# Performance work log

Hardware: AMD Instinct MI355X
Metric: run time of the kernel (lower is better)

Reference implementation:

```python
import jax, jax.numpy as jnp
import numpy as np

B, T = 64, 2048
RNN_DIM, EMB_DIM, ATTN_DIM = 1024, 512, 128
N_FILT, KSIZE = 32, 31
PAD = (KSIZE - 1) // 2


def setup_inputs() -> dict:
    key = jax.random.key(0)
    ks = jax.random.split(key, 8)
    s = 0.02
    return {
        "attention_hidden_state": jax.random.normal(ks[0], (B, RNN_DIM), jnp.float32),
        "memory": jax.random.normal(ks[1], (B, T, EMB_DIM), jnp.float32),
        "processed_memory": jax.random.normal(ks[2], (B, T, ATTN_DIM), jnp.float32),
        "attention_weights_cat": jax.random.uniform(ks[3], (B, 2, T), jnp.float32),
        "mask": jnp.zeros((B, T), dtype=bool),
        "Wq": jax.random.normal(ks[4], (ATTN_DIM, RNN_DIM), jnp.float32) * s,
        "Wconv": jax.random.normal(ks[5], (N_FILT, 2, KSIZE), jnp.float32) * s,
        "Wloc": jax.random.normal(ks[6], (ATTN_DIM, N_FILT), jnp.float32) * s,
        "Wv": jax.random.normal(ks[7], (1, ATTN_DIM), jnp.float32) * s,
    }


def reference(attention_hidden_state, memory, processed_memory,
              attention_weights_cat, mask, Wq, Wconv, Wloc, Wv):
    # query projection: [B, rnn] -> [B, 1, attn]
    pq = jnp.einsum("br,ar->ba", attention_hidden_state, Wq)[:, None, :]
    # location conv: [B, 2, T] -> [B, F, T]
    conv = jax.lax.conv_general_dilated(
        attention_weights_cat, Wconv, window_strides=(1,),
        padding=[(PAD, PAD)], dimension_numbers=("NCH", "OIH", "NCH"))
    # [B, T, F] @ Wloc.T -> [B, T, attn]
    ploc = jnp.einsum("bft,af->bta", conv, Wloc)
    # energies: [B, T]
    energies = jnp.einsum("bta,oa->bto", jnp.tanh(pq + ploc + processed_memory), Wv)[..., 0]
    alignment = jnp.where(mask, -jnp.inf, energies)
    attention_weights = jax.nn.softmax(alignment, axis=1)
    # context: [B, emb]
    attention_context = jnp.einsum("bt,bte->be", attention_weights, memory)
    return attention_context, attention_weights
```

## Files before the change

### kernel.cpp

```cpp
#include <hip/hip_runtime.h>
#include <math.h>

#define BB 64
#define TT 2048
#define RNN 1024
#define EMB 512
#define ATTN 128
#define NF 32
#define KS 31
#define PADW 15

#define TCHK_BLK 128
#define TCHK_W 32
#define NCH (TT / TCHK_W)

__device__ __forceinline__ float fast_tanh(float x) {
    float ax = fabsf(x);
    float e = __expf(-2.f * ax);
    float r = (1.f - e) * __builtin_amdgcn_rcpf(1.f + e);
    return copysignf(r, x);
}

__global__ __launch_bounds__(256) void pq_kernel(const float* __restrict__ h,
                                                 const float* __restrict__ Wq,
                                                 float* __restrict__ pq) {
    int b = blockIdx.x >> 2;
    int q = blockIdx.x & 3;
    __shared__ float s_h[RNN];
    for (int i = threadIdx.x; i < RNN; i += 256) s_h[i] = h[b * RNN + i];
    __syncthreads();

    int wave = threadIdx.x >> 6;
    int lane = threadIdx.x & 63;
#pragma unroll 2
    for (int j = 0; j < 8; ++j) {
        int a = q * 32 + wave * 8 + j;
        const float4* wq4 = (const float4*)(Wq + (size_t)a * RNN);
        float acc = 0.f;
#pragma unroll
        for (int i = 0; i < 4; ++i) {
            float4 w4 = wq4[lane + 64 * i];
            float4 h4 = *(const float4*)(s_h + 4 * (lane + 64 * i));
            acc += w4.x * h4.x + w4.y * h4.y + w4.z * h4.z + w4.w * h4.w;
        }
#pragma unroll
        for (int off = 32; off > 0; off >>= 1) acc += __shfl_xor(acc, off, 64);
        if (lane == 0) pq[b * ATTN + a] = acc;
    }
}

__global__ __launch_bounds__(256) void fused2_kernel(
    const float* __restrict__ pm,
    const float* __restrict__ awc,
    const float* __restrict__ mem,
    const unsigned char* __restrict__ mask,
    const float* __restrict__ pq,
    const float* __restrict__ Wconv,
    const float* __restrict__ Wloc,
    const float* __restrict__ Wv,
    float* __restrict__ wp,
    float* __restrict__ ms,
    float* __restrict__ cp)
{
    int b = blockIdx.x >> 4;
    int blk = blockIdx.x & 15;
    int t0b = blk * TCHK_BLK;
    int tid = threadIdx.x;
    int w = tid >> 6;
    int l = tid & 63;
    int tpair = l >> 1;
    int ah = l & 1;
    int t_local = w * TCHK_W + tpair;
    int tg = t0b + t_local;
    int ch = blk * 4 + w;
    int t0w = t0b + w * TCHK_W;

    __shared__ float s_awc[2][TCHK_BLK + 2 * PADW + 2];
    __shared__ float s_wl[ATTN * NF];
    __shared__ float s_pq[ATTN];
    __shared__ float s_wv[ATTN];
    __shared__ float s_p[4][TCHK_W];

    for (int i = tid; i < 2 * (TCHK_BLK + 2 * PADW); i += 256) {
        int c = i / (TCHK_BLK + 2 * PADW);
        int j = i % (TCHK_BLK + 2 * PADW);
        int tgj = t0b - PADW + j;
        s_awc[c][j] = (tgj >= 0 && tgj < TT) ? awc[((size_t)b * 2 + c) * TT + tgj] : 0.f;
    }
#pragma unroll
    for (int i = 0; i < 4; ++i)
        ((float4*)s_wl)[tid + 256 * i] = ((const float4*)Wloc)[tid + 256 * i];
    if (tid < ATTN) {
        s_pq[tid] = pq[b * ATTN + tid];
        s_wv[tid] = Wv[tid];
    }
    __syncthreads();

    float c_[NF];
    {
        float aw[KS];
#pragma unroll
        for (int k = 0; k < KS; ++k) aw[k] = s_awc[0][t_local + k];
#pragma unroll
        for (int f = 0; f < NF; ++f) {
            float acc = 0.f;
#pragma unroll
            for (int k = 0; k < KS; ++k)
                acc += aw[k] * Wconv[(f * 2 + 0) * KS + k];
            c_[f] = acc;
        }
#pragma unroll
        for (int k = 0; k < KS; ++k) aw[k] = s_awc[1][t_local + k];
#pragma unroll
        for (int f = 0; f < NF; ++f) {
            float acc = c_[f];
#pragma unroll
            for (int k = 0; k < KS; ++k)
                acc += aw[k] * Wconv[(f * 2 + 1) * KS + k];
            c_[f] = acc;
        }
    }

    int a0 = ah * 64;
    const float4* pm4 = (const float4*)(pm + ((size_t)b * TT + tg) * ATTN + a0);
    float epart = 0.f;

    auto enA = [&](int a_rel, float pmc) {
        int a = a0 + a_rel;
        const float4* wl4 = (const float4*)&s_wl[a << 5];
        float v = s_pq[a] + pmc;
#pragma unroll
        for (int f4 = 0; f4 < 8; ++f4) {
            float4 wq = wl4[f4];
            v += c_[f4 * 4 + 0] * wq.x + c_[f4 * 4 + 1] * wq.y +
                 c_[f4 * 4 + 2] * wq.z + c_[f4 * 4 + 3] * wq.w;
        }
        epart += s_wv[a] * fast_tanh(v);
    };

#pragma unroll
    for (int bt = 0; bt < 4; ++bt) {
        float4 q0 = pm4[bt * 4 + 0];
        float4 q1 = pm4[bt * 4 + 1];
        float4 q2 = pm4[bt * 4 + 2];
        float4 q3 = pm4[bt * 4 + 3];
        enA(bt * 16 + 0,  q0.x); enA(bt * 16 + 1,  q0.y);
        enA(bt * 16 + 2,  q0.z); enA(bt * 16 + 3,  q0.w);
        enA(bt * 16 + 4,  q1.x); enA(bt * 16 + 5,  q1.y);
        enA(bt * 16 + 6,  q1.z); enA(bt * 16 + 7,  q1.w);
        enA(bt * 16 + 8,  q2.x); enA(bt * 16 + 9,  q2.y);
        enA(bt * 16 + 10, q2.z); enA(bt * 16 + 11, q2.w);
        enA(bt * 16 + 12, q3.x); enA(bt * 16 + 13, q3.y);
        enA(bt * 16 + 14, q3.z); enA(bt * 16 + 15, q3.w);
    }

    float e = epart + __shfl_xor(epart, 1, 64);
    if (mask[(size_t)b * TT + tg] != 0) e = -1e30f;

    float m = e;
#pragma unroll
    for (int off = 2; off < 64; off <<= 1) m = fmaxf(m, __shfl_xor(m, off, 64));
    float p = __expf(e - m);
    float s = p;
#pragma unroll
    for (int off = 2; off < 64; off <<= 1) s += __shfl_xor(s, off, 64);

    if (l == 0) {
        ms[((size_t)b * NCH + ch) * 2 + 0] = m;
        ms[((size_t)b * NCH + ch) * 2 + 1] = s;
    }
    if (ah == 0) {
        wp[(size_t)b * TT + tg] = p;
        s_p[w][tpair] = p;
    }

    float4 A0 = {0.f, 0.f, 0.f, 0.f}, A1 = {0.f, 0.f, 0.f, 0.f};
    const float4* m4 = (const float4*)(mem + ((size_t)b * TT + t0w) * EMB);
#pragma unroll 8
    for (int i = 0; i < TCHK_W; ++i) {
        float pv = s_p[w][i];
        float4 v0 = m4[(size_t)i * (EMB / 4) + l];
        float4 v1 = m4[(size_t)i * (EMB / 4) + 64 + l];
        A0.x += pv * v0.x; A0.y += pv * v0.y; A0.z += pv * v0.z; A0.w += pv * v0.w;
        A1.x += pv * v1.x; A1.y += pv * v1.y; A1.z += pv * v1.z; A1.w += pv * v1.w;
    }
    float4* cp4 = (float4*)(cp + ((size_t)b * NCH + ch) * EMB);
    cp4[l] = A0;
    cp4[64 + l] = A1;
}

__global__ __launch_bounds__(256) void combine_kernel(
    const float* __restrict__ wp, const float* __restrict__ ms,
    const float* __restrict__ cp, float* __restrict__ ctx,
    float* __restrict__ wts) {
    int b = blockIdx.x;
    int tid = threadIdx.x;
    __shared__ float s_m[NCH], s_s[NCH], s_scale[NCH];
    if (tid < NCH) {
        s_m[tid] = ms[((size_t)b * NCH + tid) * 2 + 0];
        s_s[tid] = ms[((size_t)b * NCH + tid) * 2 + 1];
    }
    __syncthreads();
    float M = -1e30f;
#pragma unroll 8
    for (int c = 0; c < NCH; ++c) M = fmaxf(M, s_m[c]);
    float S = 0.f;
#pragma unroll 8
    for (int c = 0; c < NCH; ++c) S += s_s[c] * __expf(s_m[c] - M);
    float invS = 1.f / S;
    if (tid < NCH) s_scale[tid] = __expf(s_m[tid] - M) * invS;
    __syncthreads();

    {
        float2 acc = {0.f, 0.f};
        const float2* cp2 = (const float2*)(cp + (size_t)b * NCH * EMB);
#pragma unroll 8
        for (int c = 0; c < NCH; ++c) {
            float sc = s_scale[c];
            float2 v = cp2[(size_t)c * (EMB / 2) + tid];
            acc.x += sc * v.x;
            acc.y += sc * v.y;
        }
        ((float2*)(ctx + (size_t)b * EMB))[tid] = acc;
    }
#pragma unroll
    for (int i = 0; i < 8; ++i) {
        int t = i * 256 + tid;
        wts[(size_t)b * TT + t] = wp[(size_t)b * TT + t] * s_scale[t >> 5];
    }
}

extern "C" void kernel_launch(void* const* d_in, const int* in_sizes, int n_in,
                              void* d_out, int out_size, void* d_ws, size_t ws_size,
                              hipStream_t stream) {
    const float* h    = (const float*)d_in[0];
    const float* mem  = (const float*)d_in[1];
    const float* pmem = (const float*)d_in[2];
    const float* awc  = (const float*)d_in[3];
    const unsigned char* mask = (const unsigned char*)d_in[4];
    const float* Wq   = (const float*)d_in[5];
    const float* Wcv  = (const float*)d_in[6];
    const float* Wloc = (const float*)d_in[7];
    const float* Wv   = (const float*)d_in[8];

    float* out = (float*)d_out;
    float* ctx = out;
    float* wts = out + BB * EMB;

    float* ws = (float*)d_ws;
    float* pq = ws;
    float* wp = pq + BB * ATTN;
    float* ms = wp + BB * TT;
    float* cp = ms + BB * NCH * 2;

    pq_kernel<<<BB * 4, 256, 0, stream>>>(h, Wq, pq);
    fused2_kernel<<<BB * 16, 256, 0, stream>>>(pmem, awc, mem, mask, pq, Wcv,
                                               Wloc, Wv, wp, ms, cp);
    combine_kernel<<<BB, 256, 0, stream>>>(wp, ms, cp, ctx, wts);
}
```

Measured before the change: 129.7 us.

## Split conv and location projection cooperatively via shared memory with smaller chunks

The fused kernel now handles 32 timesteps per block instead of 128. It runs the location conv and the Wloc projection as separate cooperative stages through shared memory, rather than having each thread pair redundantly compute all 32 conv filters in registers. Energies are then computed with lanes spread across the attention dimension, so processed_memory loads are coalesced, and each wave reduces 8 timesteps with shuffles. Softmax chunks shrink to 8 timesteps, which makes the partial-context workspace four times larger. That raises global write and read traffic and the combine kernel's loop count, in exchange for removing duplicated ALU work and register pressure.

```diff
diff --git a/kernel.cpp b/kernel.cpp
--- a/kernel.cpp
+++ b/kernel.cpp
@@ -10,9 +10,9 @@
 #define KS 31
 #define PADW 15
 
-#define TCHK_BLK 128
-#define TCHK_W 32
-#define NCH (TT / TCHK_W)
+#define TIL 32
+#define CHT 8
+#define NCH (TT / CHT)
 
 __device__ __forceinline__ float fast_tanh(float x) {
     float ax = fabsf(x);
@@ -49,7 +49,7 @@
     }
 }
 
-__global__ __launch_bounds__(256) void fused2_kernel(
+__global__ __launch_bounds__(256) void fused3_kernel(
     const float* __restrict__ pm,
     const float* __restrict__ awc,
     const float* __restrict__ mem,
@@ -62,123 +62,140 @@
     float* __restrict__ ms,
     float* __restrict__ cp)
 {
-    int b = blockIdx.x >> 4;
-    int blk = blockIdx.x & 15;
-    int t0b = blk * TCHK_BLK;
+    int b = blockIdx.x >> 6;
+    int blk = blockIdx.x & 63;
+    int t0 = blk * TIL;
     int tid = threadIdx.x;
     int w = tid >> 6;
     int l = tid & 63;
-    int tpair = l >> 1;
-    int ah = l & 1;
-    int t_local = w * TCHK_W + tpair;
-    int tg = t0b + t_local;
-    int ch = blk * 4 + w;
-    int t0w = t0b + w * TCHK_W;
-
-    __shared__ float s_awc[2][TCHK_BLK + 2 * PADW + 2];
-    __shared__ float s_wl[ATTN * NF];
+
+    __shared__ __align__(16) float s_ploc[TIL][ATTN];
+    __shared__ __align__(16) float s_conv[TIL][40];
+    __shared__ float s_awc[2][TIL + 2 * PADW + 2];
     __shared__ float s_pq[ATTN];
     __shared__ float s_wv[ATTN];
-    __shared__ float s_p[4][TCHK_W];
-
-    for (int i = tid; i < 2 * (TCHK_BLK + 2 * PADW); i += 256) {
-        int c = i / (TCHK_BLK + 2 * PADW);
-        int j = i % (TCHK_BLK + 2 * PADW);
-        int tgj = t0b - PADW + j;
-        s_awc[c][j] = (tgj >= 0 && tgj < TT) ? awc[((size_t)b * 2 + c) * TT + tgj] : 0.f;
-    }
-#pragma unroll
-    for (int i = 0; i < 4; ++i)
-        ((float4*)s_wl)[tid + 256 * i] = ((const float4*)Wloc)[tid + 256 * i];
+
+    for (int i = tid; i < 2 * (TIL + 2 * PADW); i += 256) {
+        int c = i / (TIL + 2 * PADW);
+        int j = i % (TIL + 2 * PADW);
+        int tg = t0 - PADW + j;
+        s_awc[c][j] = (tg >= 0 && tg < TT) ? awc[((size_t)b * 2 + c) * TT + tg] : 0.f;
+    }
     if (tid < ATTN) {
         s_pq[tid] = pq[b * ATTN + tid];
         s_wv[tid] = Wv[tid];
     }
     __syncthreads();
 
-    float c_[NF];
-    {
-        float aw[KS];
-#pragma unroll
-        for (int k = 0; k < KS; ++k) aw[k] = s_awc[0][t_local + k];
-#pragma unroll
-        for (int f = 0; f < NF; ++f) {
-            float acc = 0.f;
-#pragma unroll
-            for (int k = 0; k < KS; ++k)
-                acc += aw[k] * Wconv[(f * 2 + 0) * KS + k];
-            c_[f] = acc;
-        }
-#pragma unroll
-        for (int k = 0; k < KS; ++k) aw[k] = s_awc[1][t_local + k];
-#pragma unroll
-        for (int f = 0; f < NF; ++f) {
-            float acc = c_[f];
-#pragma unroll
-            for (int k = 0; k < KS; ++k)
-                acc += aw[k] * Wconv[(f * 2 + 1) * KS + k];
-            c_[f] = acc;
-        }
-    }
-
-    int a0 = ah * 64;
-    const float4* pm4 = (const float4*)(pm + ((size_t)b * TT + tg) * ATTN + a0);
-    float epart = 0.f;
-
-    auto enA = [&](int a_rel, float pmc) {
-        int a = a0 + a_rel;
-        const float4* wl4 = (const float4*)&s_wl[a << 5];
-        float v = s_pq[a] + pmc;
-#pragma unroll
-        for (int f4 = 0; f4 < 8; ++f4) {
-            float4 wq = wl4[f4];
-            v += c_[f4 * 4 + 0] * wq.x + c_[f4 * 4 + 1] * wq.y +
-                 c_[f4 * 4 + 2] * wq.z + c_[f4 * 4 + 3] * wq.w;
-        }
-        epart += s_wv[a] * fast_tanh(v);
-    };
-
-#pragma unroll
-    for (int bt = 0; bt < 4; ++bt) {
-        float4 q0 = pm4[bt * 4 + 0];
-        float4 q1 = pm4[bt * 4 + 1];
-        float4 q2 = pm4[bt * 4 + 2];
-        float4 q3 = pm4[bt * 4 + 3];
-        enA(bt * 16 + 0,  q0.x); enA(bt * 16 + 1,  q0.y);
-        enA(bt * 16 + 2,  q0.z); enA(bt * 16 + 3,  q0.w);
-        enA(bt * 16 + 4,  q1.x); enA(bt * 16 + 5,  q1.y);
-        enA(bt * 16 + 6,  q1.z); enA(bt * 16 + 7,  q1.w);
-        enA(bt * 16 + 8,  q2.x); enA(bt * 16 + 9,  q2.y);
-        enA(bt * 16 + 10, q2.z); enA(bt * 16 + 11, q2.w);
-        enA(bt * 16 + 12, q3.x); enA(bt * 16 + 13, q3.y);
-        enA(bt * 16 + 14, q3.z); enA(bt * 16 + 15, q3.w);
-    }
-
-    float e = epart + __shfl_xor(epart, 1, 64);
-    if (mask[(size_t)b * TT + tg] != 0) e = -1e30f;
-
-    float m = e;
-#pragma unroll
-    for (int off = 2; off < 64; off <<= 1) m = fmaxf(m, __shfl_xor(m, off, 64));
-    float p = __expf(e - m);
-    float s = p;
-#pragma unroll
-    for (int off = 2; off < 64; off <<= 1) s += __shfl_xor(s, off, 64);
-
+    {
+        int t = tid & 31;
+        int fq = tid >> 5;
+        float a0 = 0.f, a1 = 0.f, a2 = 0.f, a3 = 0.f;
+#pragma unroll
+        for (int c = 0; c < 2; ++c) {
+            const float* wc = Wconv + (size_t)((fq * 4) * 2 + c) * KS;
+#pragma unroll
+            for (int k = 0; k < KS; ++k) {
+                float av = s_awc[c][t + k];
+                a0 += av * wc[k];
+                a1 += av * wc[2 * KS + k];
+                a2 += av * wc[4 * KS + k];
+                a3 += av * wc[6 * KS + k];
+            }
+        }
+        s_conv[t][fq * 4 + 0] = a0;
+        s_conv[t][fq * 4 + 1] = a1;
+        s_conv[t][fq * 4 + 2] = a2;
+        s_conv[t][fq * 4 + 3] = a3;
+    }
+    __syncthreads();
+
+    {
+        int a = tid & 127;
+        int tg = tid >> 7;
+        const float4* wlr = (const float4*)(Wloc + (size_t)a * NF);
+        float4 w0 = wlr[0], w1 = wlr[1], w2 = wlr[2], w3 = wlr[3];
+        float4 w4 = wlr[4], w5 = wlr[5], w6 = wlr[6], w7 = wlr[7];
+#pragma unroll
+        for (int tt = 0; tt < 16; ++tt) {
+            int t = tg * 16 + tt;
+            const float4* cv = (const float4*)&s_conv[t][0];
+            float4 c0 = cv[0], c1 = cv[1], c2 = cv[2], c3 = cv[3];
+            float4 c4 = cv[4], c5 = cv[5], c6 = cv[6], c7 = cv[7];
+            float acc;
+            acc  = c0.x * w0.x + c0.y * w0.y + c0.z * w0.z + c0.w * w0.w;
+            acc += c1.x * w1.x + c1.y * w1.y + c1.z * w1.z + c1.w * w1.w;
+            acc += c2.x * w2.x + c2.y * w2.y + c2.z * w2.z + c2.w * w2.w;
+            acc += c3.x * w3.x + c3.y * w3.y + c3.z * w3.z + c3.w * w3.w;
+            acc += c4.x * w4.x + c4.y * w4.y + c4.z * w4.z + c4.w * w4.w;
+            acc += c5.x * w5.x + c5.y * w5.y + c5.z * w5.z + c5.w * w5.w;
+            acc += c6.x * w6.x + c6.y * w6.y + c6.z * w6.z + c6.w * w6.w;
+            acc += c7.x * w7.x + c7.y * w7.y + c7.z * w7.z + c7.w * w7.w;
+            s_ploc[t][a] = acc;
+        }
+    }
+    __syncthreads();
+
+    float pq0 = s_pq[l], pq1 = s_pq[l + 64];
+    float wv0 = s_wv[l], wv1 = s_wv[l + 64];
+
+    float pA[CHT], pB[CHT];
+#pragma unroll
+    for (int i = 0; i < CHT; ++i) {
+        const float* r = pm + ((size_t)b * TT + t0 + w * CHT + i) * ATTN;
+        pA[i] = r[l];
+        pB[i] = r[l + 64];
+    }
+    float e[CHT];
+#pragma unroll
+    for (int i = 0; i < CHT; ++i) {
+        int t = w * CHT + i;
+        float v0 = pq0 + pA[i] + s_ploc[t][l];
+        float v1 = pq1 + pB[i] + s_ploc[t][l + 64];
+        e[i] = wv0 * fast_tanh(v0) + wv1 * fast_tanh(v1);
+    }
+#pragma unroll
+    for (int off = 32; off > 0; off >>= 1)
+#pragma unroll
+        for (int i = 0; i < CHT; ++i) e[i] += __shfl_xor(e[i], off, 64);
+
+    {
+        const unsigned int* mk = (const unsigned int*)(mask + (size_t)b * TT + t0 + w * CHT);
+        unsigned int m0 = mk[0], m1 = mk[1];
+#pragma unroll
+        for (int j = 0; j < 4; ++j) {
+            if ((m0 >> (8 * j)) & 0xff) e[j] = -1e30f;
+            if ((m1 >> (8 * j)) & 0xff) e[4 + j] = -1e30f;
+        }
+    }
+
+    float m = e[0];
+#pragma unroll
+    for (int i = 1; i < CHT; ++i) m = fmaxf(m, e[i]);
+    float p[CHT], s = 0.f;
+#pragma unroll
+    for (int i = 0; i < CHT; ++i) {
+        p[i] = __expf(e[i] - m);
+        s += p[i];
+    }
+    int ch = blk * 4 + w;
     if (l == 0) {
         ms[((size_t)b * NCH + ch) * 2 + 0] = m;
         ms[((size_t)b * NCH + ch) * 2 + 1] = s;
     }
-    if (ah == 0) {
-        wp[(size_t)b * TT + tg] = p;
-        s_p[w][tpair] = p;
+    {
+        float pv = p[0];
+#pragma unroll
+        for (int i = 1; i < CHT; ++i)
+            if (l == i) pv = p[i];
+        if (l < CHT) wp[(size_t)b * TT + t0 + w * CHT + l] = pv;
     }
 
     float4 A0 = {0.f, 0.f, 0.f, 0.f}, A1 = {0.f, 0.f, 0.f, 0.f};
-    const float4* m4 = (const float4*)(mem + ((size_t)b * TT + t0w) * EMB);
-#pragma unroll 8
-    for (int i = 0; i < TCHK_W; ++i) {
-        float pv = s_p[w][i];
+    const float4* m4 = (const float4*)(mem + ((size_t)b * TT + t0 + w * CHT) * EMB);
+#pragma unroll
+    for (int i = 0; i < CHT; ++i) {
+        float pv = p[i];
         float4 v0 = m4[(size_t)i * (EMB / 4) + l];
         float4 v1 = m4[(size_t)i * (EMB / 4) + 64 + l];
         A0.x += pv * v0.x; A0.y += pv * v0.y; A0.z += pv * v0.z; A0.w += pv * v0.w;
@@ -226,7 +243,7 @@
 #pragma unroll
     for (int i = 0; i < 8; ++i) {
         int t = i * 256 + tid;
-        wts[(size_t)b * TT + t] = wp[(size_t)b * TT + t] * s_scale[t >> 5];
+        wts[(size_t)b * TT + t] = wp[(size_t)b * TT + t] * s_scale[t >> 3];
     }
 }
 
@@ -254,7 +271,7 @@
     float* cp = ms + BB * NCH * 2;
 
     pq_kernel<<<BB * 4, 256, 0, stream>>>(h, Wq, pq);
-    fused2_kernel<<<BB * 16, 256, 0, stream>>>(pmem, awc, mem, mask, pq, Wcv,
+    fused3_kernel<<<BB * 64, 256, 0, stream>>>(pmem, awc, mem, mask, pq, Wcv,
                                                Wloc, Wv, wp, ms, cp);
     combine_kernel<<<BB, 256, 0, stream>>>(wp, ms, cp, ctx, wts);
 }
```

After: 131.6 us. About the same (+1.4%).
